# Optimization experiments

Hardware: AMD Instinct MI355X
Metric: run time of the kernel (lower is better)

## Reference

```python
import jax, jax.numpy as jnp
import numpy as np

S, XD, C, R = 6, 3, 8, 64   # num_freqs, x_dim, num_channels, res_scale
N = 262144
STD = 0.001


def setup_inputs() -> dict:
    key = jax.random.key(0)
    k1, k2, k3 = jax.random.split(key, 3)
    x = jax.random.uniform(k1, (N, XD), dtype=jnp.float32)
    features = jax.random.normal(k2, (S, 2 * XD, C, R, R), dtype=jnp.float32) * STD
    features_2d = jax.random.normal(k3, (S, 2 * XD, C, R, R), dtype=jnp.float32) * STD
    return {"x": x, "features": features, "features_2d": features_2d}


def _bilinear(img, gx, gy):
    # img: [C,H,W]; gx,gy: [P] normalized coords in [-1,1]
    # bilinear grid_sample, align_corners=True, clamped (border) indices
    _, H, W = img.shape
    ix = (gx + 1.0) * 0.5 * (W - 1)
    iy = (gy + 1.0) * 0.5 * (H - 1)
    ix0f = jnp.floor(ix)
    iy0f = jnp.floor(iy)
    wx = ix - ix0f
    wy = iy - iy0f
    ix0 = jnp.clip(ix0f.astype(jnp.int32), 0, W - 1)
    iy0 = jnp.clip(iy0f.astype(jnp.int32), 0, H - 1)
    ix1 = jnp.clip(ix0 + 1, 0, W - 1)
    iy1 = jnp.clip(iy0 + 1, 0, H - 1)
    v00 = img[:, iy0, ix0]  # [C,P]
    v01 = img[:, iy0, ix1]
    v10 = img[:, iy1, ix0]
    v11 = img[:, iy1, ix1]
    return (v00 * (1 - wx) * (1 - wy) + v01 * wx * (1 - wy)
            + v10 * (1 - wx) * wy + v11 * wx * wy)


def reference(x, features, features_2d):
    n = x.shape[0]
    scales = 2.0 ** jnp.arange(S, dtype=x.dtype)                   # [S]
    xb = x[:, None, :] * scales[:, None]                           # [N,S,3]
    latent = jnp.sin(jnp.stack([xb, xb + 0.5 * jnp.pi], axis=-2))  # [N,S,2,3]

    B = S * 2 * XD  # 36 independent (scale, sin/cos, dim) lookups

    # 1D (line) lookup: grid x-coord fixed at 0, y-coord = encoded value
    gy = jnp.transpose(latent.reshape(n, S, 2 * XD), (1, 2, 0)).reshape(B, n)
    gx = jnp.zeros_like(gy)
    fs = jax.vmap(_bilinear)(features.reshape(B, C, R, R), gx, gy)  # [B,C,N]
    fs = fs.reshape(S, 2, XD, C, n)

    # 2D (plane) lookup with cyclic dim pairs (1,2),(2,0),(0,1)
    pairs = jnp.array([[1, 2], [2, 0], [0, 1]])
    g2 = latent[..., pairs]                                        # [N,S,2,3,2]
    gx2 = jnp.transpose(g2[..., 0], (1, 2, 3, 0)).reshape(B, n)
    gy2 = jnp.transpose(g2[..., 1], (1, 2, 3, 0)).reshape(B, n)
    fs2 = jax.vmap(_bilinear)(features_2d.reshape(B, C, R, R), gx2, gy2)
    fs2 = fs2.reshape(S, 2, XD, C, n)

    out = jnp.transpose(fs * fs2, (4, 3, 0, 1, 2))                 # [N,C,S,2,3]
    out = out + latent[:, None]                                    # + PE, broadcast over C
    return out.reshape(n, C * S * 2 * XD)                          # [N, 288]
```

## Files before the change

kernel.cpp:

```cpp
#include <hip/hip_runtime.h>

#define NS 6
#define NXD 3
#define NC 8
#define NR 64
#define NB 36
#define NPOINTS 262144
#define OUTD 288
#define PTS 32

__device__ __forceinline__ unsigned short f2bf(float f) {
    unsigned u = __float_as_uint(f);
    unsigned r = u + 0x7fffu + ((u >> 16) & 1u);
    return (unsigned short)(r >> 16);
}
__device__ __forceinline__ unsigned pack2(float a, float b) {
    return (unsigned)f2bf(a) | ((unsigned)f2bf(b) << 16);
}

#define QSCALE 8192.0f
#define QINV   (1.0f / 8192.0f)

__device__ __forceinline__ unsigned f2q8(float f) {
    float q = rintf(f * QSCALE);
    q = fminf(fmaxf(q, -127.0f), 127.0f);
    return (unsigned)((int)q) & 0xffu;
}

__global__ void build_pxq(const float* __restrict__ F2, unsigned* __restrict__ px) {
    int tid = blockIdx.x * 256 + threadIdx.x;
    const int total = NB * 64 * 64 * NC;
    if (tid >= total) return;
    int c  = tid & 7;
    int xx = (tid >> 3) & 63;
    int y  = (tid >> 9) & 63;
    int b  = tid >> 15;
    const float* img = F2 + (size_t)(b * NC + c) * (NR * NR);
    int x1 = xx < 63 ? xx + 1 : 63;
    int y1 = y  < 63 ? y  + 1 : 63;
    unsigned q00 = f2q8(img[y  * NR + xx]);
    unsigned q01 = f2q8(img[y  * NR + x1]);
    unsigned q10 = f2q8(img[y1 * NR + xx]);
    unsigned q11 = f2q8(img[y1 * NR + x1]);
    px[tid] = q00 | (q01 << 8) | (q10 << 16) | (q11 << 24);
}

__global__ void build_f1q(const float* __restrict__ F, unsigned* __restrict__ f1q) {
    int tid = blockIdx.x * 256 + threadIdx.x;
    const int total = NB * 64 * NC;
    if (tid >= total) return;
    int c = tid & 7;
    int y = (tid >> 3) & 63;
    int b = tid >> 9;
    const float* img = F + (size_t)(b * NC + c) * NR * NR;
    const float sc = 0.5f * QINV;
    float a = sc * (img[y * NR + 31] + img[y * NR + 32]);
    int y1 = y < 63 ? y + 1 : 63;
    float bb = sc * (img[y1 * NR + 31] + img[y1 * NR + 32]);
    f1q[tid] = pack2(a, bb);
}

__global__ __launch_bounds__(256, 4) void encode_kernel(
    const float* __restrict__ x,
    const unsigned* __restrict__ px,
    const unsigned* __restrict__ f1q,
    float* __restrict__ out)
{
    __shared__ float stage[PTS * 289];
    const int t  = threadIdx.x;
    const int c2 = t & 3;
    const int h  = (t >> 2) & 1;
    const int u  = t >> 3;
    const int n  = blockIdx.x * PTS + u;

    const float xv0 = x[3 * n + 0];
    const float xv1 = x[3 * n + 1];
    const float xv2 = x[3 * n + 2];

    const float scb = h ? 8.0f : 1.0f;
    const float a0v = xv0 * scb, a1v = xv1 * scb, a2v = xv2 * scb;

    const int hb = 18 * h;
    const unsigned* f1p = f1q + hb * 512 + 2 * c2;
    const unsigned* pxp = px  + hb * 32768 + 2 * c2;
    float* stg = &stage[u * 289 + (2 * c2) * 36];

    #pragma unroll
    for (int gg = 0; gg < 6; ++gg) {
        const float m = (float)(1 << (gg >> 1));
        float l0, l1, l2;
        if ((gg & 1) == 0) {
            l0 = __sinf(a0v * m); l1 = __sinf(a1v * m); l2 = __sinf(a2v * m);
        } else {
            l0 = __cosf(a0v * m); l1 = __cosf(a1v * m); l2 = __cosf(a2v * m);
        }
        #pragma unroll
        for (int k = 0; k < 3; ++k) {
            const int bloc = 3 * gg + k;
            float gy1 = (k == 0) ? l0 : (k == 1) ? l1 : l2;
            float ga  = (k == 0) ? l1 : (k == 1) ? l2 : l0;
            float gb  = (k == 0) ? l2 : (k == 1) ? l0 : l1;

            float fy  = fmaxf(__builtin_fmaf(gy1, 31.5f, 31.5f), 0.0f);
            float fy0 = floorf(fy);
            float wy  = fy - fy0;
            int   y0  = (int)fy0;
            uint2 pr  = *(const uint2*)(f1p + bloc * 512 + y0 * 8);

            float fx2  = fmaxf(__builtin_fmaf(ga, 31.5f, 31.5f), 0.0f);
            float fy2  = fmaxf(__builtin_fmaf(gb, 31.5f, 31.5f), 0.0f);
            float fx20 = floorf(fx2);
            float fy20 = floorf(fy2);
            float wx2  = fx2 - fx20;
            float wy2  = fy2 - fy20;
            int   xx   = (int)fx20;
            int   yy   = (int)fy20;
            uint2 w    = *(const uint2*)(pxp + bloc * 32768 + yy * 512 + xx * 8);

            {
                float a0 = __uint_as_float(pr.x << 16);
                float a1 = __uint_as_float(pr.x & 0xffff0000u);
                float fsv = __builtin_fmaf(a1 - a0, wy, a0);
                float v00 = (float)((int)(w.x << 24) >> 24);
                float v01 = (float)((int)(w.x << 16) >> 24);
                float v10 = (float)((int)(w.x <<  8) >> 24);
                float v11 = (float)((int)w.x        >> 24);
                float tp = __builtin_fmaf(v01 - v00, wx2, v00);
                float bt = __builtin_fmaf(v11 - v10, wx2, v10);
                float fs2v = __builtin_fmaf(bt - tp, wy2, tp);
                stg[hb + bloc] = __builtin_fmaf(fsv, fs2v, gy1);
            }
            {
                float a0 = __uint_as_float(pr.y << 16);
                float a1 = __uint_as_float(pr.y & 0xffff0000u);
                float fsv = __builtin_fmaf(a1 - a0, wy, a0);
                float v00 = (float)((int)(w.y << 24) >> 24);
                float v01 = (float)((int)(w.y << 16) >> 24);
                float v10 = (float)((int)(w.y <<  8) >> 24);
                float v11 = (float)((int)w.y        >> 24);
                float tp = __builtin_fmaf(v01 - v00, wx2, v00);
                float bt = __builtin_fmaf(v11 - v10, wx2, v10);
                float fs2v = __builtin_fmaf(bt - tp, wy2, tp);
                stg[36 + hb + bloc] = __builtin_fmaf(fsv, fs2v, gy1);
            }
        }
    }
    __syncthreads();

    float* ob = out + (size_t)blockIdx.x * (PTS * OUTD);
    #pragma unroll
    for (int r = 0; r < 36; ++r) {
        int e = t + r * 256;
        int uu = e / 288;
        int v = e - uu * 288;
        ob[e] = stage[uu * 289 + v];
    }
}

extern "C" void kernel_launch(void* const* d_in, const int* in_sizes, int n_in,
                              void* d_out, int out_size, void* d_ws, size_t ws_size,
                              hipStream_t stream)
{
    const float* x  = (const float*)d_in[0];
    const float* F  = (const float*)d_in[1];
    const float* F2 = (const float*)d_in[2];
    float* out = (float*)d_out;

    unsigned* px  = (unsigned*)d_ws;
    unsigned* f1q = px + NB * 64 * 64 * NC;

    build_pxq<<<(NB * 64 * 64 * NC + 255) / 256, 256, 0, stream>>>(F2, px);
    build_f1q<<<(NB * 64 * NC + 255) / 256, 256, 0, stream>>>(F, f1q);
    encode_kernel<<<NPOINTS / PTS, 256, 0, stream>>>(x, px, f1q, out);
}
```

Before: 370.9 us.

## Split encode work to one channel per thread with 512-thread blocks

Each thread now handles a single channel instead of two, so blocks double to 512 threads and each thread does 4-byte gathers instead of 8-byte uint2 gathers. The aim is more parallelism and lower per-thread register pressure, which helps hide gather latency. In exchange, the sin/cos and coordinate math is recomputed twice as often across threads, and there are more, narrower memory transactions.

Measured after the change: 380.9 us. +2.7%, slower.

```diff
diff --git a/kernel.cpp b/kernel.cpp
--- a/kernel.cpp
+++ b/kernel.cpp
@@ -60,7 +60,7 @@
     f1q[tid] = pack2(a, bb);
 }
 
-__global__ __launch_bounds__(256, 4) void encode_kernel(
+__global__ __launch_bounds__(512, 6) void encode_kernel(
     const float* __restrict__ x,
     const unsigned* __restrict__ px,
     const unsigned* __restrict__ f1q,
@@ -68,22 +68,22 @@
 {
     __shared__ float stage[PTS * 289];
     const int t  = threadIdx.x;
-    const int c2 = t & 3;
-    const int h  = (t >> 2) & 1;
-    const int u  = t >> 3;
+    const int hh = t & 1;
+    const int c  = (t >> 1) & 7;
+    const int u  = t >> 4;
     const int n  = blockIdx.x * PTS + u;
 
     const float xv0 = x[3 * n + 0];
     const float xv1 = x[3 * n + 1];
     const float xv2 = x[3 * n + 2];
 
-    const float scb = h ? 8.0f : 1.0f;
+    const float scb = hh ? 8.0f : 1.0f;
     const float a0v = xv0 * scb, a1v = xv1 * scb, a2v = xv2 * scb;
 
-    const int hb = 18 * h;
-    const unsigned* f1p = f1q + hb * 512 + 2 * c2;
-    const unsigned* pxp = px  + hb * 32768 + 2 * c2;
-    float* stg = &stage[u * 289 + (2 * c2) * 36];
+    const int hb = 18 * hh;
+    const unsigned* f1p = f1q + hb * 512 + c;
+    const unsigned* pxp = px  + hb * 32768 + c;
+    float* stg = &stage[u * 289 + c * 36 + hb];
 
     #pragma unroll
     for (int gg = 0; gg < 6; ++gg) {
@@ -96,7 +96,7 @@
         }
         #pragma unroll
         for (int k = 0; k < 3; ++k) {
-            const int bloc = 3 * gg + k;
+            const int bl = 3 * gg + k;
             float gy1 = (k == 0) ? l0 : (k == 1) ? l1 : l2;
             float ga  = (k == 0) ? l1 : (k == 1) ? l2 : l0;
             float gb  = (k == 0) ? l2 : (k == 1) ? l0 : l1;
@@ -105,7 +105,7 @@
             float fy0 = floorf(fy);
             float wy  = fy - fy0;
             int   y0  = (int)fy0;
-            uint2 pr  = *(const uint2*)(f1p + bloc * 512 + y0 * 8);
+            unsigned pr = f1p[bl * 512 + y0 * 8];
 
             float fx2  = fmaxf(__builtin_fmaf(ga, 31.5f, 31.5f), 0.0f);
             float fy2  = fmaxf(__builtin_fmaf(gb, 31.5f, 31.5f), 0.0f);
@@ -115,42 +115,29 @@
             float wy2  = fy2 - fy20;
             int   xx   = (int)fx20;
             int   yy   = (int)fy20;
-            uint2 w    = *(const uint2*)(pxp + bloc * 32768 + yy * 512 + xx * 8);
+            unsigned w = pxp[bl * 32768 + yy * 512 + xx * 8];
 
-            {
-                float a0 = __uint_as_float(pr.x << 16);
-                float a1 = __uint_as_float(pr.x & 0xffff0000u);
-                float fsv = __builtin_fmaf(a1 - a0, wy, a0);
-                float v00 = (float)((int)(w.x << 24) >> 24);
-                float v01 = (float)((int)(w.x << 16) >> 24);
-                float v10 = (float)((int)(w.x <<  8) >> 24);
-                float v11 = (float)((int)w.x        >> 24);
-                float tp = __builtin_fmaf(v01 - v00, wx2, v00);
-                float bt = __builtin_fmaf(v11 - v10, wx2, v10);
-                float fs2v = __builtin_fmaf(bt - tp, wy2, tp);
-                stg[hb + bloc] = __builtin_fmaf(fsv, fs2v, gy1);
-            }
-            {
-                float a0 = __uint_as_float(pr.y << 16);
-                float a1 = __uint_as_float(pr.y & 0xffff0000u);
-                float fsv = __builtin_fmaf(a1 - a0, wy, a0);
-                float v00 = (float)((int)(w.y << 24) >> 24);
-                float v01 = (float)((int)(w.y << 16) >> 24);
-                float v10 = (float)((int)(w.y <<  8) >> 24);
-                float v11 = (float)((int)w.y        >> 24);
-                float tp = __builtin_fmaf(v01 - v00, wx2, v00);
-                float bt = __builtin_fmaf(v11 - v10, wx2, v10);
-                float fs2v = __builtin_fmaf(bt - tp, wy2, tp);
-                stg[36 + hb + bloc] = __builtin_fmaf(fsv, fs2v, gy1);
-            }
+            float a0 = __uint_as_float(pr << 16);
+            float a1 = __uint_as_float(pr & 0xffff0000u);
+            float fsv = __builtin_fmaf(a1 - a0, wy, a0);
+
+            float v00 = (float)((int)(w << 24) >> 24);
+            float v01 = (float)((int)(w << 16) >> 24);
+            float v10 = (float)((int)(w <<  8) >> 24);
+            float v11 = (float)((int)w        >> 24);
+            float tp = __builtin_fmaf(v01 - v00, wx2, v00);
+            float bt = __builtin_fmaf(v11 - v10, wx2, v10);
+            float fs2v = __builtin_fmaf(bt - tp, wy2, tp);
+
+            stg[bl] = __builtin_fmaf(fsv, fs2v, gy1);
         }
     }
     __syncthreads();
 
     float* ob = out + (size_t)blockIdx.x * (PTS * OUTD);
     #pragma unroll
-    for (int r = 0; r < 36; ++r) {
-        int e = t + r * 256;
+    for (int r = 0; r < 18; ++r) {
+        int e = t + r * 512;
         int uu = e / 288;
         int v = e - uu * 288;
         ob[e] = stage[uu * 289 + v];
@@ -171,5 +158,5 @@
 
     build_pxq<<<(NB * 64 * 64 * NC + 255) / 256, 256, 0, stream>>>(F2, px);
     build_f1q<<<(NB * 64 * NC + 255) / 256, 256, 0, stream>>>(F, f1q);
-    encode_kernel<<<NPOINTS / PTS, 256, 0, stream>>>(x, px, f1q, out);
+    encode_kernel<<<NPOINTS / PTS, 512, 0, stream>>>(x, px, f1q, out);
 }
```
